# Performance work log

Hardware: AMD Instinct MI355X
Metric: run time of the kernel (lower is better)

The kernel has to match this reference:

```python
import jax, jax.numpy as jnp
import numpy as np

K, N = 1024, 16384


def setup_inputs() -> dict:
    key = jax.random.key(0)
    k0, k1, k2 = jax.random.split(key, 3)
    # event counts (non-negative), like the COVID case-count observations
    obs = jax.random.uniform(k0, (K, N), dtype=jnp.float32) * 10.0
    # Beta ~ U(1, 3), Alpha ~ U(0, 0.01) per the torch parameter init
    Beta = 1.0 + 2.0 * jax.random.uniform(k1, (K,), dtype=jnp.float32)
    Alpha = 0.01 * jax.random.uniform(k2, (K, K), dtype=jnp.float32)
    return {"obs": obs, "Beta": Beta, "Alpha": Alpha}


def reference(obs, Beta, Alpha):
    """Hawkes log-likelihood, exact O(N*K) recursion replacing the O(N^2*K^2) loop.

    Original per-step math (t > 0):
      lam1[k, t] = softplus( sum_j Alpha[k, j] * sum_{tp < t} obs[j, tp] * Beta[j] * exp(-(t - tp) * Beta[j]) )
    The exponential kernel gives S_{t+1} = exp(-Beta) * (S_t + obs[:, t]), S_0 = 0,
    where S_t[j] = sum_{tp < t} obs[j, tp] * exp(-(t - tp) * Beta[j]).
    lam1[:, 0] = 0 exactly (the torch code returns zeros at t = 0, not softplus(0)).
    """
    Mu0 = obs.mean(axis=1) / 10.0 + 1e-5                      # [K] background rate
    decay = jnp.exp(-Beta)                                    # [K]

    def step(S, o_t):                                         # S: [K], o_t: [K]
        return decay * (S + o_t), S                           # emit S_t, carry S_{t+1}

    _, S_seq = jax.lax.scan(step, jnp.zeros_like(Beta), obs.T)  # S_seq: [N, K]

    G = Beta[None, :] * S_seq                                 # [N, K] = Beta_j * S_t[j]
    lam1 = jax.nn.softplus(G @ Alpha.T).T                     # [K, N]; row k = softplus(Alpha @ g_t)
    lam1 = lam1.at[:, 0].set(0.0)                             # t = 0 branch returns zeros

    lams0 = jnp.broadcast_to(Mu0[:, None], obs.shape)         # [K, N]
    Nloglams = obs * jnp.log(lams0 + lam1 + 1e-5)
    loglik = (Nloglams - lams0 - lam1).sum()
    return loglik, lams0, lam1
```

## Files before the change

### kernel.cpp

```cpp
#include <hip/hip_runtime.h>
#include <hip/hip_bf16.h>
#include <stdint.h>

#define K_DIM 1024
#define N_DIM 16384

typedef __attribute__((ext_vector_type(4))) float floatx4;

__device__ __forceinline__ void async_copy16(const void* g, void* l) {
  __builtin_amdgcn_global_load_lds((const __attribute__((address_space(1))) void*)g,
                                   (__attribute__((address_space(3))) void*)l,
                                   16, 0, 0);
}

__device__ __forceinline__ int pk4_e4m3(float a, float b, float c, float d) {
  int lo = __builtin_amdgcn_cvt_pk_fp8_f32(a, b, 0, false);
  return __builtin_amdgcn_cvt_pk_fp8_f32(c, d, lo, true);
}

#define A_SCALE 512.0f
#define G_SCALE 32.0f
#define INV_SCALE (1.0f / (512.0f * 32.0f))

__global__ __launch_bounds__(256) void mu_convert(const float* __restrict__ obs,
                                                  const float* __restrict__ Alpha,
                                                  float* __restrict__ mu_acc,
                                                  int* __restrict__ A8) {
  const int k = blockIdx.x;
  const int tid = threadIdx.x;
  const float* row = obs + (size_t)k * N_DIM;
  float s = 0.f;
  for (int t = tid * 4; t < N_DIM; t += 256 * 4) {
    float4 v = *(const float4*)(row + t);
    s += (v.x + v.y) + (v.z + v.w);
  }
  #pragma unroll
  for (int off = 32; off > 0; off >>= 1) s += __shfl_down(s, off);
  __shared__ float ws[4];
  if ((tid & 63) == 0) ws[tid >> 6] = s;
  float4 av = *(const float4*)(Alpha + (size_t)k * K_DIM + tid * 4);
  A8[k * 256 + tid] = pk4_e4m3(av.x * A_SCALE, av.y * A_SCALE, av.z * A_SCALE, av.w * A_SCALE);
  __syncthreads();
  if (tid == 0) mu_acc[k] = (ws[0] + ws[1]) + (ws[2] + ws[3]);
}

__global__ __launch_bounds__(256) void scan_kernel(const float* __restrict__ obs,
                                                   const float* __restrict__ Beta,
                                                   unsigned char* __restrict__ Gt8) {
  __shared__ float tile[64][161];
  const int tw = blockIdx.x;
  const int jg = blockIdx.y;
  const int j0 = jg * 64;
  const int t0 = tw * 128;
  const int tid = threadIdx.x;

  for (int u = tid; u < 64 * 40; u += 256) {
    int row = u / 40;
    int c4 = u % 40;
    int tloc = c4 * 4;
    int tg = t0 - 32 + tloc;
    float4 v;
    if (tg >= 0) {
      v = *(const float4*)(obs + (size_t)(j0 + row) * N_DIM + tg);
    } else {
      v = make_float4(0.f, 0.f, 0.f, 0.f);
    }
    tile[row][tloc]     = v.x;
    tile[row][tloc + 1] = v.y;
    tile[row][tloc + 2] = v.z;
    tile[row][tloc + 3] = v.w;
  }
  __syncthreads();

  const int w = tid >> 6;
  const int lane = tid & 63;
  const int j = j0 + lane;
  const float beta = Beta[j];
  const float decay = __expf(-beta);
  const int lt0 = w * 32;
  float S = 0.f;
  #pragma unroll
  for (int i = 0; i < 32; ++i) S = decay * (S + tile[lane][lt0 + i]);
  const int tg = t0 + w * 32;
  #pragma unroll
  for (int i = 0; i < 32; ++i) {
    int p = __builtin_amdgcn_cvt_pk_fp8_f32(G_SCALE * beta * S, 0.f, 0, false);
    Gt8[(size_t)(tg + i) * K_DIM + j] = (unsigned char)(p & 0xff);
    S = decay * (S + tile[lane][lt0 + 32 + i]);
  }
}

__global__ __launch_bounds__(256) void gemm_kernel(const unsigned char* __restrict__ A8,
                                                   const unsigned char* __restrict__ B8,
                                                   const float* __restrict__ obs,
                                                   const float* __restrict__ mu_acc,
                                                   float* __restrict__ lam1_out,
                                                   float* __restrict__ lams0_out,
                                                   double* __restrict__ acc_out) {
  const int tb = blockIdx.x;
  const int kb = blockIdx.y;
  const int tid = threadIdx.x;
  const int lane = tid & 63, w = tid >> 6;
  const int wm = w >> 1, wn = w & 1;
  const int ml = lane & 15, q = lane >> 4;

  __shared__ unsigned char As[128 * 64];
  __shared__ unsigned char Bs[128 * 64];
  __shared__ float wsum[4];

  floatx4 acc[4][4] = {};

  const unsigned char* Ab = A8 + (size_t)kb * 128 * K_DIM;
  const unsigned char* Bb = B8 + (size_t)tb * 128 * K_DIM;

  for (int kt = 0; kt < 16; ++kt) {
    const unsigned char* Ak = Ab + kt * 64;
    const unsigned char* Bk = Bb + kt * 64;
    #pragma unroll
    for (int it = 0; it < 2; ++it) {
      int L = it * 256 + tid;
      int r = L >> 2;
      int c = L & 3;
      int cg = c ^ ((r >> 1) & 3);
      async_copy16(Ak + (size_t)r * K_DIM + cg * 16, &As[L * 16]);
      async_copy16(Bk + (size_t)r * K_DIM + cg * 16, &Bs[L * 16]);
    }
    __syncthreads();

    #pragma unroll
    for (int kk = 0; kk < 2; ++kk) {
      long a[4], b[4];
      const int c0 = kk * 2 + (q >> 1);
      const int sub = (q & 1) * 8;
      #pragma unroll
      for (int mf = 0; mf < 4; ++mf) {
        int r = wm * 64 + mf * 16 + ml;
        int cg = c0 ^ ((r >> 1) & 3);
        a[mf] = *(const long*)&As[r * 64 + cg * 16 + sub];
      }
      #pragma unroll
      for (int nf = 0; nf < 4; ++nf) {
        int r = wn * 64 + nf * 16 + ml;
        int cg = c0 ^ ((r >> 1) & 3);
        b[nf] = *(const long*)&Bs[r * 64 + cg * 16 + sub];
      }
      #pragma unroll
      for (int mf = 0; mf < 4; ++mf)
        #pragma unroll
        for (int nf = 0; nf < 4; ++nf)
          acc[mf][nf] = __builtin_amdgcn_mfma_f32_16x16x32_fp8_fp8(a[mf], b[nf], acc[mf][nf], 0, 0, 0);
    }
    __syncthreads();
  }

  float lsum = 0.f;
  const int kblk = kb * 128 + wm * 64;
  const int tblk = tb * 128 + wn * 64;
  #pragma unroll
  for (int mf = 0; mf < 4; ++mf) {
    int k4 = kblk + mf * 16 + q * 4;
    floatx4 mu4 = *(const floatx4*)&mu_acc[k4];
    #pragma unroll
    for (int r = 0; r < 4; ++r) {
      int k = k4 + r;
      float mu = mu4[r] * (1.0f / 163840.0f) + 1e-5f;
      #pragma unroll
      for (int nf = 0; nf < 4; ++nf) {
        int t = tblk + nf * 16 + ml;
        float raw = acc[mf][nf][r] * INV_SCALE;
        float e = __expf(-fabsf(raw));
        float lam = fmaxf(raw, 0.f) + __logf(1.f + e);
        if (t == 0) lam = 0.f;
        lam1_out[(size_t)k * N_DIM + t] = lam;
        if (lams0_out) lams0_out[(size_t)k * N_DIM + t] = mu;
        float o = obs[(size_t)k * N_DIM + t];
        lsum += o * __logf(mu + lam + 1e-5f) - mu - lam;
      }
    }
  }
  #pragma unroll
  for (int off = 32; off > 0; off >>= 1) lsum += __shfl_down(lsum, off);
  if (lane == 0) wsum[w] = lsum;
  __syncthreads();
  if (tid == 0) atomicAdd(acc_out, (double)(wsum[0] + wsum[1] + wsum[2] + wsum[3]));
}

__global__ void tail_kernel(const double* __restrict__ acc, float* __restrict__ out) {
  out[0] = (float)(*acc);
}

__global__ __launch_bounds__(256) void finalize_kernel(const float* __restrict__ mu_acc,
                                                       const double* __restrict__ acc,
                                                       float* __restrict__ out) {
  int k = blockIdx.x;
  float mu = mu_acc[k] * (1.0f / 163840.0f) + 1e-5f;
  float* dst = out + 1 + (size_t)k * N_DIM;
  int tid = threadIdx.x;
  if (tid < 3) dst[tid] = mu;
  float4 v4 = make_float4(mu, mu, mu, mu);
  for (int t = 3 + tid * 4; t + 3 < N_DIM; t += 256 * 4) *(float4*)(dst + t) = v4;
  if (tid == 3) dst[N_DIM - 1] = mu;
  if (blockIdx.x == 0 && tid == 4) out[0] = (float)(*acc);
}

extern "C" void kernel_launch(void* const* d_in, const int* in_sizes, int n_in,
                              void* d_out, int out_size, void* d_ws, size_t ws_size,
                              hipStream_t stream) {
  const float* obs   = (const float*)d_in[0];
  const float* Beta  = (const float*)d_in[1];
  const float* Alpha = (const float*)d_in[2];
  float* out = (float*)d_out;

  double* acc   = (double*)d_ws;
  float* mu_acc = (float*)((char*)d_ws + 16);

  const bool ws_big = ws_size >= (size_t)(8192 + 17 * 1024 * 1024 + 4096);
  unsigned char* Gt8;
  unsigned char* A8;
  if (ws_big) {
    Gt8 = (unsigned char*)d_ws + 8192;
    A8  = Gt8 + (size_t)N_DIM * K_DIM;
  } else {
    Gt8 = (unsigned char*)(out + 4);
    A8  = Gt8 + (size_t)N_DIM * K_DIM;
  }

  hipMemsetAsync(d_ws, 0, 16, stream);

  mu_convert<<<dim3(K_DIM), 256, 0, stream>>>(obs, Alpha, mu_acc, (int*)A8);

  scan_kernel<<<dim3(N_DIM / 128, K_DIM / 64), 256, 0, stream>>>(obs, Beta, Gt8);

  gemm_kernel<<<dim3(N_DIM / 128, K_DIM / 128), 256, 0, stream>>>(
      A8, Gt8, obs, mu_acc,
      out + 1 + (size_t)K_DIM * N_DIM,
      ws_big ? (out + 1) : nullptr,
      acc);

  if (ws_big) {
    tail_kernel<<<1, 1, 0, stream>>>(acc, out);
  } else {
    finalize_kernel<<<dim3(K_DIM), 256, 0, stream>>>(mu_acc, acc, out);
  }
}
```

Baseline: 287.3 us.

## Fuse obs row-sum into scan kernel and deepen GEMM K-tile to 128

```diff
diff --git a/kernel.cpp b/kernel.cpp
--- a/kernel.cpp
+++ b/kernel.cpp
@@ -22,31 +22,17 @@
 #define G_SCALE 32.0f
 #define INV_SCALE (1.0f / (512.0f * 32.0f))
 
-__global__ __launch_bounds__(256) void mu_convert(const float* __restrict__ obs,
-                                                  const float* __restrict__ Alpha,
-                                                  float* __restrict__ mu_acc,
-                                                  int* __restrict__ A8) {
-  const int k = blockIdx.x;
-  const int tid = threadIdx.x;
-  const float* row = obs + (size_t)k * N_DIM;
-  float s = 0.f;
-  for (int t = tid * 4; t < N_DIM; t += 256 * 4) {
-    float4 v = *(const float4*)(row + t);
-    s += (v.x + v.y) + (v.z + v.w);
-  }
-  #pragma unroll
-  for (int off = 32; off > 0; off >>= 1) s += __shfl_down(s, off);
-  __shared__ float ws[4];
-  if ((tid & 63) == 0) ws[tid >> 6] = s;
-  float4 av = *(const float4*)(Alpha + (size_t)k * K_DIM + tid * 4);
-  A8[k * 256 + tid] = pk4_e4m3(av.x * A_SCALE, av.y * A_SCALE, av.z * A_SCALE, av.w * A_SCALE);
-  __syncthreads();
-  if (tid == 0) mu_acc[k] = (ws[0] + ws[1]) + (ws[2] + ws[3]);
+__global__ __launch_bounds__(256) void convert_alpha(const float* __restrict__ A,
+                                                     int* __restrict__ A8) {
+  int idx = blockIdx.x * 256 + threadIdx.x;
+  float4 v = *(const float4*)(A + (size_t)idx * 4);
+  A8[idx] = pk4_e4m3(v.x * A_SCALE, v.y * A_SCALE, v.z * A_SCALE, v.w * A_SCALE);
 }
 
 __global__ __launch_bounds__(256) void scan_kernel(const float* __restrict__ obs,
                                                    const float* __restrict__ Beta,
-                                                   unsigned char* __restrict__ Gt8) {
+                                                   unsigned char* __restrict__ Gt8,
+                                                   float* __restrict__ mu_acc) {
   __shared__ float tile[64][161];
   const int tw = blockIdx.x;
   const int jg = blockIdx.y;
@@ -72,6 +58,15 @@
   }
   __syncthreads();
 
+  {
+    int row = tid & 63;
+    int qq = tid >> 6;
+    float s = 0.f;
+    #pragma unroll 8
+    for (int i = 0; i < 32; ++i) s += tile[row][32 + qq * 32 + i];
+    atomicAdd(&mu_acc[j0 + row], s);
+  }
+
   const int w = tid >> 6;
   const int lane = tid & 63;
   const int j = j0 + lane;
@@ -90,13 +85,13 @@
   }
 }
 
-__global__ __launch_bounds__(256) void gemm_kernel(const unsigned char* __restrict__ A8,
-                                                   const unsigned char* __restrict__ B8,
-                                                   const float* __restrict__ obs,
-                                                   const float* __restrict__ mu_acc,
-                                                   float* __restrict__ lam1_out,
-                                                   float* __restrict__ lams0_out,
-                                                   double* __restrict__ acc_out) {
+__global__ __launch_bounds__(256, 4) void gemm_kernel(const unsigned char* __restrict__ A8,
+                                                      const unsigned char* __restrict__ B8,
+                                                      const float* __restrict__ obs,
+                                                      const float* __restrict__ mu_acc,
+                                                      float* __restrict__ lam1_out,
+                                                      float* __restrict__ lams0_out,
+                                                      double* __restrict__ acc_out) {
   const int tb = blockIdx.x;
   const int kb = blockIdx.y;
   const int tid = threadIdx.x;
@@ -104,8 +99,8 @@
   const int wm = w >> 1, wn = w & 1;
   const int ml = lane & 15, q = lane >> 4;
 
-  __shared__ unsigned char As[128 * 64];
-  __shared__ unsigned char Bs[128 * 64];
+  __shared__ unsigned char As[128 * 128];
+  __shared__ unsigned char Bs[128 * 128];
   __shared__ float wsum[4];
 
   floatx4 acc[4][4] = {};
@@ -113,36 +108,36 @@
   const unsigned char* Ab = A8 + (size_t)kb * 128 * K_DIM;
   const unsigned char* Bb = B8 + (size_t)tb * 128 * K_DIM;
 
-  for (int kt = 0; kt < 16; ++kt) {
-    const unsigned char* Ak = Ab + kt * 64;
-    const unsigned char* Bk = Bb + kt * 64;
+  for (int kt = 0; kt < 8; ++kt) {
+    const unsigned char* Ak = Ab + kt * 128;
+    const unsigned char* Bk = Bb + kt * 128;
     #pragma unroll
-    for (int it = 0; it < 2; ++it) {
+    for (int it = 0; it < 4; ++it) {
       int L = it * 256 + tid;
-      int r = L >> 2;
-      int c = L & 3;
-      int cg = c ^ ((r >> 1) & 3);
+      int r = L >> 3;
+      int c = L & 7;
+      int cg = c ^ (r & 7);
       async_copy16(Ak + (size_t)r * K_DIM + cg * 16, &As[L * 16]);
       async_copy16(Bk + (size_t)r * K_DIM + cg * 16, &Bs[L * 16]);
     }
     __syncthreads();
 
     #pragma unroll
-    for (int kk = 0; kk < 2; ++kk) {
+    for (int kk = 0; kk < 4; ++kk) {
       long a[4], b[4];
       const int c0 = kk * 2 + (q >> 1);
       const int sub = (q & 1) * 8;
       #pragma unroll
       for (int mf = 0; mf < 4; ++mf) {
         int r = wm * 64 + mf * 16 + ml;
-        int cg = c0 ^ ((r >> 1) & 3);
-        a[mf] = *(const long*)&As[r * 64 + cg * 16 + sub];
+        int cg = c0 ^ (r & 7);
+        a[mf] = *(const long*)&As[r * 128 + cg * 16 + sub];
       }
       #pragma unroll
       for (int nf = 0; nf < 4; ++nf) {
         int r = wn * 64 + nf * 16 + ml;
-        int cg = c0 ^ ((r >> 1) & 3);
-        b[nf] = *(const long*)&Bs[r * 64 + cg * 16 + sub];
+        int cg = c0 ^ (r & 7);
+        b[nf] = *(const long*)&Bs[r * 128 + cg * 16 + sub];
       }
       #pragma unroll
       for (int mf = 0; mf < 4; ++mf)
@@ -225,11 +220,11 @@
     A8  = Gt8 + (size_t)N_DIM * K_DIM;
   }
 
-  hipMemsetAsync(d_ws, 0, 16, stream);
-
-  mu_convert<<<dim3(K_DIM), 256, 0, stream>>>(obs, Alpha, mu_acc, (int*)A8);
-
-  scan_kernel<<<dim3(N_DIM / 128, K_DIM / 64), 256, 0, stream>>>(obs, Beta, Gt8);
+  hipMemsetAsync(d_ws, 0, 16 + K_DIM * sizeof(float), stream);
+
+  convert_alpha<<<dim3(K_DIM * K_DIM / (256 * 4)), 256, 0, stream>>>(Alpha, (int*)A8);
+
+  scan_kernel<<<dim3(N_DIM / 128, K_DIM / 64), 256, 0, stream>>>(obs, Beta, Gt8, mu_acc);
 
   gemm_kernel<<<dim3(N_DIM / 128, K_DIM / 128), 256, 0, stream>>>(
       A8, Gt8, obs, mu_acc,
```

After: 328.5 us. 14.3% more time.
